# Kernel optimization log

Measured on AMD Instinct MI355X. Metric: run time of the kernel, lower is better.

The kernel has to match this reference:

```python
import jax, jax.numpy as jnp
import numpy as np

UNITS = 2048
RHO = 0.99          # spectral_radius
LEAKY = 1.0         # leaky integration coefficient
INPUT_SCALING = 1.0
BIAS_SCALING = 1.0
B, T, D_IN = 32, 512, 128


def setup_inputs() -> dict:
    key = jax.random.key(0)
    k1, k2, k3 = jax.random.split(key, 3)
    inputs = jax.random.normal(k1, (B, T, D_IN), dtype=jnp.float32)
    h0 = jnp.zeros((B, UNITS), dtype=jnp.float32)
    # original uses deterministic +/-1 signs from pi digits; same structure: sign matrix * scaling
    kernel = jnp.where(jax.random.uniform(k2, (D_IN, UNITS)) >= 0.5, 1.0, -1.0).astype(jnp.float32) * INPUT_SCALING
    bias = jnp.where(jax.random.uniform(k3, (UNITS,)) >= 0.5, 1.0, -1.0).astype(jnp.float32) * BIAS_SCALING
    return {"inputs": inputs, "h0": h0, "kernel": kernel, "bias": bias}


def reference(inputs, h0, kernel, bias):
    # Precompute input projection for all timesteps: [B, T, U]
    u = jnp.einsum("btd,du->btu", inputs, kernel)

    def step(h, u_t):
        # prev @ recurrent_kernel == spectral_radius * cyclic shift of prev
        state_part = RHO * jnp.roll(h, 1, axis=-1)
        h_new = h * (1.0 - LEAKY) + jnp.tanh(u_t + bias + state_part) * LEAKY
        return h_new, h_new

    _, ys = jax.lax.scan(step, h0, jnp.swapaxes(u, 0, 1))  # scan over time
    return jnp.swapaxes(ys, 0, 1)  # [B, T, U]
```

## Files before the change

kernel.cpp:

```cpp
#include <hip/hip_runtime.h>
#include <hip/hip_bf16.h>

#define U_ 2048
#define T_ 512
#define K_ 128
#define B_ 32
#define RHO_ 0.99f
#define CPB 128
#define NTILES 9
#define NSLOTS 10

typedef __attribute__((ext_vector_type(8))) short short8;
typedef __attribute__((ext_vector_type(4))) float f32x4;

__device__ __forceinline__ float fast_tanh(float x) {
  float e = __expf(2.0f * x);
  return 1.0f - 2.0f / (e + 1.0f);
}

__device__ __forceinline__ unsigned short bf16_rne(float x) {
  unsigned int u = __float_as_uint(x);
  u += 0x7FFFu + ((u >> 16) & 1u);
  return (unsigned short)(u >> 16);
}

__global__ __launch_bounds__(256) void convert_a_kernel(
    const float* __restrict__ A, unsigned short* __restrict__ Ab) {
  const int gi = blockIdx.x * 256 + threadIdx.x;
  const int m = gi >> 5;
  const int kq = (gi & 31) << 2;
  const float4 v = *(const float4*)&A[(size_t)m * K_ + kq];
  ushort4 hi, lo;
  hi.x = bf16_rne(v.x); hi.y = bf16_rne(v.y); hi.z = bf16_rne(v.z); hi.w = bf16_rne(v.w);
  lo.x = bf16_rne(v.x - __uint_as_float((unsigned)hi.x << 16));
  lo.y = bf16_rne(v.y - __uint_as_float((unsigned)hi.y << 16));
  lo.z = bf16_rne(v.z - __uint_as_float((unsigned)hi.z << 16));
  lo.w = bf16_rne(v.w - __uint_as_float((unsigned)hi.w << 16));
  *(ushort4*)&Ab[(size_t)m * 256 + kq] = hi;
  *(ushort4*)&Ab[(size_t)m * 256 + 128 + kq] = lo;
}

__global__ __launch_bounds__(256) void convert_w_kernel(
    const float* __restrict__ W, unsigned short* __restrict__ Wbt) {
  const int gi = blockIdx.x * 256 + threadIdx.x;
  const int kq = gi >> 11;
  const int n = gi & 2047;
  const int k = kq << 2;
  ushort4 w;
  w.x = bf16_rne(W[(size_t)(k + 0) * U_ + n]);
  w.y = bf16_rne(W[(size_t)(k + 1) * U_ + n]);
  w.z = bf16_rne(W[(size_t)(k + 2) * U_ + n]);
  w.w = bf16_rne(W[(size_t)(k + 3) * U_ + n]);
  *(ushort4*)&Wbt[(size_t)n * 256 + k] = w;
  *(ushort4*)&Wbt[(size_t)n * 256 + 128 + k] = w;
}

__global__ __launch_bounds__(256, 2) void fused_gemm_scan2_kernel(
    const unsigned short* __restrict__ Ab, const unsigned short* __restrict__ Wbt,
    const float* __restrict__ bias, const float* __restrict__ h0,
    float* __restrict__ out) {
  __shared__ unsigned short Wl[NSLOTS * 2048];
  __shared__ float u_lds[16 * 146];
  __shared__ float bias_lds[U_];
  const int tid = threadIdx.x;
  const int id = blockIdx.x + (blockIdx.y << 4);
  const int xcd = id & 7;
  const int wk = id >> 3;
  const int b = (xcd << 2) + (wk >> 4);
  const int bx = wk & 15;
  const int c0 = bx << 7;
  const int cbase = bx << 3;
  const int wave = tid >> 6;
  const int lane = tid & 63;
  const int r = lane & 15;
  const int q = lane >> 4;
  const int koff = q << 3;
  const int nloc = tid >> 4;
  const int gran = tid & 15;
  const int sgran = gran ^ (nloc & 7);

  #pragma unroll
  for (int i = 0; i < 8; ++i)
    bias_lds[(i << 8) + tid] = bias[(i << 8) + tid];

  #pragma unroll
  for (int j = 0; j < NTILES; ++j) {
    const int g = (cbase + j) & 127;
    const short8 w0 = *(const short8*)(Wbt + ((((size_t)g << 4) + nloc) << 8) + (gran << 3));
    *(short8*)&Wl[(j << 11) + (nloc << 7) + (sgran << 3)] = w0;
  }

  const unsigned short* const aBase = Ab + (((size_t)b * T_) << 8);
  short8 af[8];
  #pragma unroll
  for (int ks = 0; ks < 8; ++ks)
    af[ks] = *(const short8*)(aBase + (((size_t)r) << 8) + (ks << 5) + koff);

  float h = 0.0f;
  if (tid < CPB)
    h = h0[((size_t)b << 11) + ((c0 + tid + U_ - 1) & (U_ - 1))];

  __syncthreads();

  for (int it = 0; it < T_ / 16; ++it) {
    const int t0 = it << 4;

    short8 wv;
    if (it + 1 < T_ / 16) {
      const int gnew = (cbase + it + NTILES) & 127;
      wv = *(const short8*)(Wbt + ((((size_t)gnew << 4) + nloc) << 8) + (gran << 3));
    }

    f32x4 acc[3];
    #pragma unroll
    for (int u = 0; u < 3; ++u) {
      acc[u] = (f32x4){0.f, 0.f, 0.f, 0.f};
      const int j = (u < 2) ? (wave + (u << 2)) : 8;
      if (u < 2 || wave == 0) {
        const int slot = (it + j) % NSLOTS;
        short8 bfk[4];
        #pragma unroll
        for (int ks = 0; ks < 4; ++ks)
          bfk[ks] = *(const short8*)&Wl[(slot << 11) + (r << 7) +
                                        ((((ks << 2) + q) ^ (r & 7)) << 3)];
        #pragma unroll
        for (int ks = 0; ks < 8; ++ks)
          acc[u] = __builtin_amdgcn_mfma_f32_16x16x32_bf16(af[ks], bfk[ks & 3], acc[u], 0, 0, 0);
      }
    }

    __syncthreads();

    #pragma unroll
    for (int u = 0; u < 3; ++u) {
      const int j = (u < 2) ? (wave + (u << 2)) : 8;
      if (u < 2 || wave == 0) {
        const float bv = bias_lds[(c0 + t0 + (j << 4) + r) & (U_ - 1)];
        #pragma unroll
        for (int reg = 0; reg < 4; ++reg)
          u_lds[((q << 2) + reg) * 146 + (j << 4) + r] = acc[u][reg] + bv;
      }
    }

    if (it + 1 < T_ / 16) {
      #pragma unroll
      for (int ks = 0; ks < 8; ++ks)
        af[ks] = *(const short8*)(aBase + (((size_t)(t0 + 16 + r)) << 8) + (ks << 5) + koff);
      const int snew = (it + NTILES) % NSLOTS;
      *(short8*)&Wl[(snew << 11) + (nloc << 7) + (sgran << 3)] = wv;
    }

    __syncthreads();

    if (tid < CPB) {
      float uv[16];
      #pragma unroll
      for (int tt = 0; tt < 16; ++tt)
        uv[tt] = u_lds[tt * 146 + tid + tt];
      float* const orow = out + (((size_t)(b * T_ + t0)) << 11);
      #pragma unroll
      for (int tt = 0; tt < 16; ++tt) {
        h = fast_tanh(fmaf(RHO_, h, uv[tt]));
        __builtin_nontemporal_store(
            h, &orow[((size_t)tt << 11) + ((c0 + tid + t0 + tt) & (U_ - 1))]);
      }
    }
  }
}

__global__ __launch_bounds__(256) void ring_scan_kernel(
    float* __restrict__ buf, const float* __restrict__ h0) {
  const int b = blockIdx.y;
  const int c = (blockIdx.x << 8) + threadIdx.x;
  float* const base = buf + (size_t)b * (T_ * U_);
  float h = h0[((size_t)b << 11) + ((c + U_ - 1) & (U_ - 1))];
  float wA[8], wB[8];
  #pragma unroll
  for (int j = 0; j < 8; ++j)
    wA[j] = base[((size_t)j << 11) + ((c + j) & (U_ - 1))];
  for (int t0 = 0; t0 < T_; t0 += 16) {
    #pragma unroll
    for (int j = 0; j < 8; ++j) {
      const int t = t0 + 8 + j;
      wB[j] = base[((size_t)t << 11) + ((c + t) & (U_ - 1))];
    }
    #pragma unroll
    for (int j = 0; j < 8; ++j) {
      const int t = t0 + j;
      h = fast_tanh(fmaf(RHO_, h, wA[j]));
      base[((size_t)t << 11) + ((c + t) & (U_ - 1))] = h;
    }
    if (t0 + 16 < T_) {
      #pragma unroll
      for (int j = 0; j < 8; ++j) {
        const int t = t0 + 16 + j;
        wA[j] = base[((size_t)t << 11) + ((c + t) & (U_ - 1))];
      }
    }
    #pragma unroll
    for (int j = 0; j < 8; ++j) {
      const int t = t0 + 8 + j;
      h = fast_tanh(fmaf(RHO_, h, wB[j]));
      base[((size_t)t << 11) + ((c + t) & (U_ - 1))] = h;
    }
  }
}

__global__ __launch_bounds__(256, 4) void gemm_bias_kernel(
    const float* __restrict__ A, const float* __restrict__ W,
    const float* __restrict__ bias, float* __restrict__ out) {
  __shared__ float Asf[64][68];
  __shared__ float Bsf[64][64];
  const int tid = threadIdx.x;
  const int m0 = blockIdx.y << 6;
  const int n0 = blockIdx.x << 6;
  const int tx = tid & 15;
  const int ty = tid >> 4;
  float acc[4][4] = {};
  #pragma unroll
  for (int kb = 0; kb < 2; ++kb) {
    if (kb) __syncthreads();
    {
      const int c4 = tid & 15;
      const int r0 = tid >> 4;
      #pragma unroll
      for (int rr = 0; rr < 4; ++rr) {
        const int r = r0 + (rr << 4);
        const float4 v = *(const float4*)(A + (size_t)(m0 + r) * K_ + (kb << 6) + (c4 << 2));
        Asf[(c4 << 2) + 0][r] = v.x;
        Asf[(c4 << 2) + 1][r] = v.y;
        Asf[(c4 << 2) + 2][r] = v.z;
        Asf[(c4 << 2) + 3][r] = v.w;
      }
    }
    {
      const int c4 = tid & 15;
      const int r0 = tid >> 4;
      #pragma unroll
      for (int rr = 0; rr < 4; ++rr) {
        const int k = r0 + (rr << 4);
        *(float4*)&Bsf[k][c4 << 2] =
            *(const float4*)(W + (size_t)((kb << 6) + k) * U_ + n0 + (c4 << 2));
      }
    }
    __syncthreads();
    #pragma unroll 16
    for (int k = 0; k < 64; ++k) {
      const float4 a = *(const float4*)&Asf[k][ty << 2];
      const float4 b = *(const float4*)&Bsf[k][tx << 2];
      acc[0][0] = fmaf(a.x, b.x, acc[0][0]); acc[0][1] = fmaf(a.x, b.y, acc[0][1]);
      acc[0][2] = fmaf(a.x, b.z, acc[0][2]); acc[0][3] = fmaf(a.x, b.w, acc[0][3]);
      acc[1][0] = fmaf(a.y, b.x, acc[1][0]); acc[1][1] = fmaf(a.y, b.y, acc[1][1]);
      acc[1][2] = fmaf(a.y, b.z, acc[1][2]); acc[1][3] = fmaf(a.y, b.w, acc[1][3]);
      acc[2][0] = fmaf(a.z, b.x, acc[2][0]); acc[2][1] = fmaf(a.z, b.y, acc[2][1]);
      acc[2][2] = fmaf(a.z, b.z, acc[2][2]); acc[2][3] = fmaf(a.z, b.w, acc[2][3]);
      acc[3][0] = fmaf(a.w, b.x, acc[3][0]); acc[3][1] = fmaf(a.w, b.y, acc[3][1]);
      acc[3][2] = fmaf(a.w, b.z, acc[3][2]); acc[3][3] = fmaf(a.w, b.w, acc[3][3]);
    }
  }
  const float4 bv = *(const float4*)(bias + n0 + (tx << 2));
  #pragma unroll
  for (int i = 0; i < 4; ++i) {
    float4 o;
    o.x = acc[i][0] + bv.x; o.y = acc[i][1] + bv.y;
    o.z = acc[i][2] + bv.z; o.w = acc[i][3] + bv.w;
    *(float4*)(out + (size_t)(m0 + (ty << 2) + i) * U_ + n0 + (tx << 2)) = o;
  }
}

extern "C" void kernel_launch(void* const* d_in, const int* in_sizes, int n_in,
                              void* d_out, int out_size, void* d_ws, size_t ws_size,
                              hipStream_t stream) {
  const float* A    = (const float*)d_in[0];
  const float* h0   = (const float*)d_in[1];
  const float* W    = (const float*)d_in[2];
  const float* bias = (const float*)d_in[3];
  float* out = (float*)d_out;

  const size_t AB_BYTES = (size_t)B_ * T_ * 256 * 2;
  const size_t WB_BYTES = (size_t)U_ * 256 * 2;
  const size_t NEEDED = AB_BYTES + WB_BYTES;

  if (ws_size >= NEEDED) {
    unsigned short* Ab  = (unsigned short*)d_ws;
    unsigned short* Wbt = (unsigned short*)((char*)d_ws + AB_BYTES);

    convert_a_kernel<<<2048, 256, 0, stream>>>(A, Ab);
    convert_w_kernel<<<256, 256, 0, stream>>>(W, Wbt);
    dim3 fg(U_ / CPB, B_);
    fused_gemm_scan2_kernel<<<fg, 256, 0, stream>>>(Ab, Wbt, bias, h0, out);
  } else {
    dim3 gemm_grid(U_ / 64, (B_ * T_) / 64);
    gemm_bias_kernel<<<gemm_grid, 64, 0, stream>>>(A, W, bias, out);
    dim3 scan_grid(U_ / 256, B_);
    ring_scan_kernel<<<scan_grid, 256, 0, stream>>>(out, h0);
  }
}
```

Before: 221.7 us.

## Halve columns per block, drop LDS weight ring, load weights directly from global

Each block of the fused GEMM+scan kernel now owns 64 columns instead of 128, doubling the grid to 1024 blocks and raising the occupancy hint to 4 blocks per CU. The LDS ring buffer that staged weight tiles is removed; each wave now reads its bf16 weight fragments straight from global memory (expected to hit in L2) every iteration. The tanh uses raw exp2 and rcp intrinsics. Only 64 threads per block now run the serial scan. The extra parallelism across CUs comes at the cost of more global/L2 traffic for weights and more redundant GEMM work per output column. The fallback GEMM launch also changes its block size.

New measurement: 326.3 us. +47.2%, slower.

```diff
diff --git a/kernel.cpp b/kernel.cpp
--- a/kernel.cpp
+++ b/kernel.cpp
@@ -6,16 +6,15 @@
 #define K_ 128
 #define B_ 32
 #define RHO_ 0.99f
-#define CPB 128
-#define NTILES 9
-#define NSLOTS 10
+#define CPB 64
+#define NTILES 5
 
 typedef __attribute__((ext_vector_type(8))) short short8;
 typedef __attribute__((ext_vector_type(4))) float f32x4;
 
 __device__ __forceinline__ float fast_tanh(float x) {
-  float e = __expf(2.0f * x);
-  return 1.0f - 2.0f / (e + 1.0f);
+  float e = __builtin_amdgcn_exp2f(2.8853900817779268f * x);
+  return 1.0f - 2.0f * __builtin_amdgcn_rcpf(e + 1.0f);
 }
 
 __device__ __forceinline__ unsigned short bf16_rne(float x) {
@@ -55,40 +54,29 @@
   *(ushort4*)&Wbt[(size_t)n * 256 + 128 + k] = w;
 }
 
-__global__ __launch_bounds__(256, 2) void fused_gemm_scan2_kernel(
+__global__ __launch_bounds__(256, 4) void fused_gemm_scan3_kernel(
     const unsigned short* __restrict__ Ab, const unsigned short* __restrict__ Wbt,
     const float* __restrict__ bias, const float* __restrict__ h0,
     float* __restrict__ out) {
-  __shared__ unsigned short Wl[NSLOTS * 2048];
-  __shared__ float u_lds[16 * 146];
+  __shared__ float u_lds[16 * 82];
   __shared__ float bias_lds[U_];
   const int tid = threadIdx.x;
-  const int id = blockIdx.x + (blockIdx.y << 4);
+  const int id = blockIdx.x + (blockIdx.y << 5);
   const int xcd = id & 7;
   const int wk = id >> 3;
-  const int b = (xcd << 2) + (wk >> 4);
-  const int bx = wk & 15;
-  const int c0 = bx << 7;
-  const int cbase = bx << 3;
+  const int b = (xcd << 2) + (wk >> 5);
+  const int bx = wk & 31;
+  const int c0 = bx << 6;
+  const int cbase = bx << 2;
   const int wave = tid >> 6;
   const int lane = tid & 63;
   const int r = lane & 15;
   const int q = lane >> 4;
   const int koff = q << 3;
-  const int nloc = tid >> 4;
-  const int gran = tid & 15;
-  const int sgran = gran ^ (nloc & 7);
 
   #pragma unroll
   for (int i = 0; i < 8; ++i)
     bias_lds[(i << 8) + tid] = bias[(i << 8) + tid];
-
-  #pragma unroll
-  for (int j = 0; j < NTILES; ++j) {
-    const int g = (cbase + j) & 127;
-    const short8 w0 = *(const short8*)(Wbt + ((((size_t)g << 4) + nloc) << 8) + (gran << 3));
-    *(short8*)&Wl[(j << 11) + (nloc << 7) + (sgran << 3)] = w0;
-  }
 
   const unsigned short* const aBase = Ab + (((size_t)b * T_) << 8);
   short8 af[8];
@@ -105,40 +93,39 @@
   for (int it = 0; it < T_ / 16; ++it) {
     const int t0 = it << 4;
 
-    short8 wv;
-    if (it + 1 < T_ / 16) {
-      const int gnew = (cbase + it + NTILES) & 127;
-      wv = *(const short8*)(Wbt + ((((size_t)gnew << 4) + nloc) << 8) + (gran << 3));
-    }
-
-    f32x4 acc[3];
-    #pragma unroll
-    for (int u = 0; u < 3; ++u) {
-      acc[u] = (f32x4){0.f, 0.f, 0.f, 0.f};
-      const int j = (u < 2) ? (wave + (u << 2)) : 8;
-      if (u < 2 || wave == 0) {
-        const int slot = (it + j) % NSLOTS;
-        short8 bfk[4];
+    short8 bfq[2][4];
+    #pragma unroll
+    for (int u = 0; u < 2; ++u) {
+      const int j = (u == 0) ? wave : 4;
+      if (u == 0 || wave == 0) {
+        const int n = (((cbase + it + j) & 127) << 4) + r;
         #pragma unroll
         for (int ks = 0; ks < 4; ++ks)
-          bfk[ks] = *(const short8*)&Wl[(slot << 11) + (r << 7) +
-                                        ((((ks << 2) + q) ^ (r & 7)) << 3)];
+          bfq[u][ks] = *(const short8*)(Wbt + ((size_t)n << 8) + (ks << 5) + koff);
+      }
+    }
+
+    f32x4 acc[2];
+    #pragma unroll
+    for (int u = 0; u < 2; ++u) {
+      acc[u] = (f32x4){0.f, 0.f, 0.f, 0.f};
+      if (u == 0 || wave == 0) {
         #pragma unroll
         for (int ks = 0; ks < 8; ++ks)
-          acc[u] = __builtin_amdgcn_mfma_f32_16x16x32_bf16(af[ks], bfk[ks & 3], acc[u], 0, 0, 0);
+          acc[u] = __builtin_amdgcn_mfma_f32_16x16x32_bf16(af[ks], bfq[u][ks & 3], acc[u], 0, 0, 0);
       }
     }
 
     __syncthreads();
 
     #pragma unroll
-    for (int u = 0; u < 3; ++u) {
-      const int j = (u < 2) ? (wave + (u << 2)) : 8;
-      if (u < 2 || wave == 0) {
+    for (int u = 0; u < 2; ++u) {
+      const int j = (u == 0) ? wave : 4;
+      if (u == 0 || wave == 0) {
         const float bv = bias_lds[(c0 + t0 + (j << 4) + r) & (U_ - 1)];
         #pragma unroll
         for (int reg = 0; reg < 4; ++reg)
-          u_lds[((q << 2) + reg) * 146 + (j << 4) + r] = acc[u][reg] + bv;
+          u_lds[((q << 2) + reg) * 82 + (j << 4) + r] = acc[u][reg] + bv;
       }
     }
 
@@ -146,8 +133,6 @@
       #pragma unroll
       for (int ks = 0; ks < 8; ++ks)
         af[ks] = *(const short8*)(aBase + (((size_t)(t0 + 16 + r)) << 8) + (ks << 5) + koff);
-      const int snew = (it + NTILES) % NSLOTS;
-      *(short8*)&Wl[(snew << 11) + (nloc << 7) + (sgran << 3)] = wv;
     }
 
     __syncthreads();
@@ -156,7 +141,7 @@
       float uv[16];
       #pragma unroll
       for (int tt = 0; tt < 16; ++tt)
-        uv[tt] = u_lds[tt * 146 + tid + tt];
+        uv[tt] = u_lds[tt * 82 + tid + tt];
       float* const orow = out + (((size_t)(b * T_ + t0)) << 11);
       #pragma unroll
       for (int tt = 0; tt < 16; ++tt) {
@@ -288,10 +273,10 @@
     convert_a_kernel<<<2048, 256, 0, stream>>>(A, Ab);
     convert_w_kernel<<<256, 256, 0, stream>>>(W, Wbt);
     dim3 fg(U_ / CPB, B_);
-    fused_gemm_scan2_kernel<<<fg, 256, 0, stream>>>(Ab, Wbt, bias, h0, out);
+    fused_gemm_scan3_kernel<<<fg, 256, 0, stream>>>(Ab, Wbt, bias, h0, out);
   } else {
     dim3 gemm_grid(U_ / 64, (B_ * T_) / 64);
-    gemm_bias_kernel<<<gemm_grid, 64, 0, stream>>>(A, W, bias, out);
+    gemm_bias_kernel<<<gemm_grid, 256, 0, stream>>>(A, W, bias, out);
     dim3 scan_grid(U_ / 256, B_);
     ring_scan_kernel<<<scan_grid, 256, 0, stream>>>(out, h0);
   }
```

## Stream A and W tiles via direct global-to-LDS loads with double-buffered u tile

Applied to the files above, without the earlier changes.

Replaces register-staged loads of A fragments and W tiles with global_load_lds into a swizzled, double-buffered LDS area. The u tile is double-buffered so one __syncthreads per iteration is removed, and bias moves from a staged LDS array to register prefetch. fast_tanh now uses the native exp2 and rcp intrinsics. The aim is to overlap the next tile's memory traffic with the MFMA and scan work and to cut barrier count, at the cost of more LDS use and relying on async-load ordering. The fallback path's gemm launch block size also changes from 64 to 256, which may not match that kernel's expectations.

Result: faster. 192.7 us (-13.1%).

```diff
diff --git a/kernel.cpp b/kernel.cpp
--- a/kernel.cpp
+++ b/kernel.cpp
@@ -14,8 +14,8 @@
 typedef __attribute__((ext_vector_type(4))) float f32x4;
 
 __device__ __forceinline__ float fast_tanh(float x) {
-  float e = __expf(2.0f * x);
-  return 1.0f - 2.0f / (e + 1.0f);
+  float e = __builtin_amdgcn_exp2f(2.8853900817779268f * x);
+  return 1.0f - 2.0f * __builtin_amdgcn_rcpf(e + 1.0f);
 }
 
 __device__ __forceinline__ unsigned short bf16_rne(float x) {
@@ -23,6 +23,11 @@
   u += 0x7FFFu + ((u >> 16) & 1u);
   return (unsigned short)(u >> 16);
 }
+
+#define GLOAD_LDS16(gsrc, ldst)                                        \
+  __builtin_amdgcn_global_load_lds(                                    \
+      (const __attribute__((address_space(1))) void*)(gsrc),           \
+      (__attribute__((address_space(3))) void*)(ldst), 16, 0, 0)
 
 __global__ __launch_bounds__(256) void convert_a_kernel(
     const float* __restrict__ A, unsigned short* __restrict__ Ab) {
@@ -55,13 +60,13 @@
   *(ushort4*)&Wbt[(size_t)n * 256 + 128 + k] = w;
 }
 
-__global__ __launch_bounds__(256, 2) void fused_gemm_scan2_kernel(
+__global__ __launch_bounds__(256, 2) void fused_gemm_scan4_kernel(
     const unsigned short* __restrict__ Ab, const unsigned short* __restrict__ Wbt,
     const float* __restrict__ bias, const float* __restrict__ h0,
     float* __restrict__ out) {
   __shared__ unsigned short Wl[NSLOTS * 2048];
-  __shared__ float u_lds[16 * 146];
-  __shared__ float bias_lds[U_];
+  __shared__ unsigned short Al[2][4096];
+  __shared__ float u_lds[2][16 * 146];
   const int tid = threadIdx.x;
   const int id = blockIdx.x + (blockIdx.y << 4);
   const int xcd = id & 7;
@@ -74,28 +79,28 @@
   const int lane = tid & 63;
   const int r = lane & 15;
   const int q = lane >> 4;
-  const int koff = q << 3;
-  const int nloc = tid >> 4;
-  const int gran = tid & 15;
-  const int sgran = gran ^ (nloc & 7);
-
-  #pragma unroll
-  for (int i = 0; i < 8; ++i)
-    bias_lds[(i << 8) + tid] = bias[(i << 8) + tid];
-
+
+  const int wrow = tid >> 4;
+  const int wlg  = (tid & 15) ^ (wrow & 7);
+  const int arow0 = tid >> 5;
+  const int alg0  = (tid & 31) ^ (arow0 & 7);
+  const int arow1 = 8 + arow0;
+  const int alg1  = (tid & 31) ^ (arow1 & 7);
+
+  const unsigned short* const aBase = Ab + (((size_t)b * T_) << 8);
+
+  GLOAD_LDS16(aBase + (((size_t)arow0) << 8) + (alg0 << 3), &Al[0][tid << 3]);
+  GLOAD_LDS16(aBase + (((size_t)arow1) << 8) + (alg1 << 3), &Al[0][(tid + 256) << 3]);
   #pragma unroll
   for (int j = 0; j < NTILES; ++j) {
     const int g = (cbase + j) & 127;
-    const short8 w0 = *(const short8*)(Wbt + ((((size_t)g << 4) + nloc) << 8) + (gran << 3));
-    *(short8*)&Wl[(j << 11) + (nloc << 7) + (sgran << 3)] = w0;
-  }
-
-  const unsigned short* const aBase = Ab + (((size_t)b * T_) << 8);
-  short8 af[8];
-  #pragma unroll
-  for (int ks = 0; ks < 8; ++ks)
-    af[ks] = *(const short8*)(aBase + (((size_t)r) << 8) + (ks << 5) + koff);
-
+    GLOAD_LDS16(Wbt + (((size_t)((g << 4) + wrow)) << 8) + (wlg << 3),
+                &Wl[(j << 11) + (tid << 3)]);
+  }
+  float bv[3], nbv[3];
+  bv[0] = bias[(c0 + (wave << 4) + r) & (U_ - 1)];
+  bv[1] = bias[(c0 + ((wave + 4) << 4) + r) & (U_ - 1)];
+  bv[2] = (wave == 0) ? bias[(c0 + 128 + r) & (U_ - 1)] : 0.0f;
   float h = 0.0f;
   if (tid < CPB)
     h = h0[((size_t)b << 11) + ((c0 + tid + U_ - 1) & (U_ - 1))];
@@ -103,18 +108,29 @@
   __syncthreads();
 
   for (int it = 0; it < T_ / 16; ++it) {
+    const int cur = it & 1;
     const int t0 = it << 4;
 
-    short8 wv;
     if (it + 1 < T_ / 16) {
-      const int gnew = (cbase + it + NTILES) & 127;
-      wv = *(const short8*)(Wbt + ((((size_t)gnew << 4) + nloc) << 8) + (gran << 3));
-    }
-
-    f32x4 acc[3];
+      GLOAD_LDS16(aBase + (((size_t)(t0 + 16 + arow0)) << 8) + (alg0 << 3),
+                  &Al[cur ^ 1][tid << 3]);
+      GLOAD_LDS16(aBase + (((size_t)(t0 + 16 + arow1)) << 8) + (alg1 << 3),
+                  &Al[cur ^ 1][(tid + 256) << 3]);
+      const int g = (cbase + it + NTILES) & 127;
+      GLOAD_LDS16(Wbt + (((size_t)((g << 4) + wrow)) << 8) + (wlg << 3),
+                  &Wl[(((it + NTILES) % NSLOTS) << 11) + (tid << 3)]);
+      nbv[0] = bias[(c0 + t0 + 16 + (wave << 4) + r) & (U_ - 1)];
+      nbv[1] = bias[(c0 + t0 + 16 + ((wave + 4) << 4) + r) & (U_ - 1)];
+      if (wave == 0) nbv[2] = bias[(c0 + t0 + 16 + 128 + r) & (U_ - 1)];
+    }
+
+    short8 af[8];
+    #pragma unroll
+    for (int ks = 0; ks < 8; ++ks)
+      af[ks] = *(const short8*)&Al[cur][(r << 8) + ((((ks << 2) + q) ^ (r & 7)) << 3)];
+
     #pragma unroll
     for (int u = 0; u < 3; ++u) {
-      acc[u] = (f32x4){0.f, 0.f, 0.f, 0.f};
       const int j = (u < 2) ? (wave + (u << 2)) : 8;
       if (u < 2 || wave == 0) {
         const int slot = (it + j) % NSLOTS;
@@ -123,31 +139,14 @@
         for (int ks = 0; ks < 4; ++ks)
           bfk[ks] = *(const short8*)&Wl[(slot << 11) + (r << 7) +
                                         ((((ks << 2) + q) ^ (r & 7)) << 3)];
+        f32x4 acc = (f32x4){0.f, 0.f, 0.f, 0.f};
         #pragma unroll
         for (int ks = 0; ks < 8; ++ks)
-          acc[u] = __builtin_amdgcn_mfma_f32_16x16x32_bf16(af[ks], bfk[ks & 3], acc[u], 0, 0, 0);
-      }
-    }
-
-    __syncthreads();
-
-    #pragma unroll
-    for (int u = 0; u < 3; ++u) {
-      const int j = (u < 2) ? (wave + (u << 2)) : 8;
-      if (u < 2 || wave == 0) {
-        const float bv = bias_lds[(c0 + t0 + (j << 4) + r) & (U_ - 1)];
+          acc = __builtin_amdgcn_mfma_f32_16x16x32_bf16(af[ks], bfk[ks & 3], acc, 0, 0, 0);
         #pragma unroll
         for (int reg = 0; reg < 4; ++reg)
-          u_lds[((q << 2) + reg) * 146 + (j << 4) + r] = acc[u][reg] + bv;
-      }
-    }
-
-    if (it + 1 < T_ / 16) {
-      #pragma unroll
-      for (int ks = 0; ks < 8; ++ks)
-        af[ks] = *(const short8*)(aBase + (((size_t)(t0 + 16 + r)) << 8) + (ks << 5) + koff);
-      const int snew = (it + NTILES) % NSLOTS;
-      *(short8*)&Wl[(snew << 11) + (nloc << 7) + (sgran << 3)] = wv;
+          u_lds[cur][((q << 2) + reg) * 146 + (j << 4) + r] = acc[reg] + bv[u];
+      }
     }
 
     __syncthreads();
@@ -156,7 +155,7 @@
       float uv[16];
       #pragma unroll
       for (int tt = 0; tt < 16; ++tt)
-        uv[tt] = u_lds[tt * 146 + tid + tt];
+        uv[tt] = u_lds[cur][tt * 146 + tid + tt];
       float* const orow = out + (((size_t)(b * T_ + t0)) << 11);
       #pragma unroll
       for (int tt = 0; tt < 16; ++tt) {
@@ -165,6 +164,7 @@
             h, &orow[((size_t)tt << 11) + ((c0 + tid + t0 + tt) & (U_ - 1))]);
       }
     }
+    bv[0] = nbv[0]; bv[1] = nbv[1]; bv[2] = nbv[2];
   }
 }
 
@@ -288,10 +288,10 @@
     convert_a_kernel<<<2048, 256, 0, stream>>>(A, Ab);
     convert_w_kernel<<<256, 256, 0, stream>>>(W, Wbt);
     dim3 fg(U_ / CPB, B_);
-    fused_gemm_scan2_kernel<<<fg, 256, 0, stream>>>(Ab, Wbt, bias, h0, out);
+    fused_gemm_scan4_kernel<<<fg, 256, 0, stream>>>(Ab, Wbt, bias, h0, out);
   } else {
     dim3 gemm_grid(U_ / 64, (B_ * T_) / 64);
-    gemm_bias_kernel<<<gemm_grid, 64, 0, stream>>>(A, W, bias, out);
+    gemm_bias_kernel<<<gemm_grid, 256, 0, stream>>>(A, W, bias, out);
     dim3 scan_grid(U_ / 256, B_);
     ring_scan_kernel<<<scan_grid, 256, 0, stream>>>(out, h0);
   }
```
